# Performance work log

Measured on AMD Instinct MI355X. Metric: run time of the kernel, lower is better.

## Reference

```python
import jax, jax.numpy as jnp
import numpy as np

N_NODES = 100000
N_EDGES = 6400000
EPS = 1e-12


def _gcn_conv(x, edge_index, W, b, n):
    # PyG GCNConv(normalize=True): add self-loops, symmetric deg^-1/2 norm
    src, dst = edge_index[0], edge_index[1]
    loop = jnp.arange(n)
    row = jnp.concatenate([src, loop])
    col = jnp.concatenate([dst, loop])
    deg = jax.ops.segment_sum(jnp.ones(row.shape[0], dtype=x.dtype), col, num_segments=n)
    dinv = jnp.where(deg > 0, jax.lax.rsqrt(deg), 0.0)
    norm = dinv[row] * dinv[col]                       # [E+N]
    xw = x @ W                                          # [N,16]
    out = jax.ops.segment_sum(xw[row] * norm[:, None], col, num_segments=n)
    return out + b


def _sage_conv(x, edge_index, Wl, bl, Wr, n):
    # PyG SAGEConv(aggr='mean', root_weight=True, normalize=True)
    src, dst = edge_index[0], edge_index[1]
    deg = jax.ops.segment_sum(jnp.ones(src.shape[0], dtype=x.dtype), dst, num_segments=n)
    agg = jax.ops.segment_sum(x[src], dst, num_segments=n) / jnp.maximum(deg, 1.0)[:, None]
    out = agg @ Wl + bl + x @ Wr
    nrm = jnp.sqrt(jnp.sum(out * out, axis=-1, keepdims=True))
    return out / jnp.maximum(nrm, EPS)                  # F.normalize(p=2)


def setup_inputs() -> dict:
    key = jax.random.key(0)
    ks = jax.random.split(key, 16)
    s16, s128 = 1.0 / np.sqrt(16.0), 1.0 / np.sqrt(128.0)
    inp = {
        "x": jax.random.normal(ks[0], (N_NODES, 16), dtype=jnp.float32),
        "edge_index": jax.random.randint(ks[1], (2, N_EDGES), 0, N_NODES, dtype=jnp.int64),
        "W_gcn": jax.random.uniform(ks[2], (16, 16), jnp.float32, -s16, s16),
        "b_gcn": jnp.zeros((16,), jnp.float32),
        "Wl1": jax.random.uniform(ks[3], (16, 16), jnp.float32, -s16, s16),
        "bl1": jnp.zeros((16,), jnp.float32),
        "Wr1": jax.random.uniform(ks[4], (16, 16), jnp.float32, -s16, s16),
        "Wl2": jax.random.uniform(ks[5], (16, 16), jnp.float32, -s16, s16),
        "bl2": jnp.zeros((16,), jnp.float32),
        "Wr2": jax.random.uniform(ks[6], (16, 16), jnp.float32, -s16, s16),
        "W1": jax.random.uniform(ks[7], (16, 128), jnp.float32, -s16, s16),
        "b1": jax.random.uniform(ks[8], (128,), jnp.float32, -s16, s16),
        "W2": jax.random.uniform(ks[9], (128, 128), jnp.float32, -s128, s128),
        "b2": jax.random.uniform(ks[10], (128,), jnp.float32, -s128, s128),
        "W3": jax.random.uniform(ks[11], (128, 1), jnp.float32, -s128, s128),
        "b3": jax.random.uniform(ks[12], (1,), jnp.float32, -s128, s128),
    }
    return inp


def reference(x, edge_index, W_gcn, b_gcn, Wl1, bl1, Wr1, Wl2, bl2, Wr2, W1, b1, W2, b2, W3, b3):
    n = x.shape[0]
    h = jnp.tanh(_gcn_conv(x, edge_index, W_gcn, b_gcn, n))
    h = jnp.tanh(_sage_conv(h, edge_index, Wl1, bl1, Wr1, n))
    h = _sage_conv(h, edge_index, Wl2, bl2, Wr2, n)
    h = jax.nn.relu(h @ W1 + b1)
    h = jax.nn.relu(h @ W2 + b2)
    return h @ W3 + b3
```

## Files before the change

kernel.cpp:

```cpp
#include <hip/hip_runtime.h>
#include <hip/hip_bf16.h>
#include <math.h>

#define NBLK 512
#define ROWS (NBLK / 256)
#define MAXNC 512
#define STAGE_CAP 12512

__global__ void k_hist(const int* __restrict__ dst, int* __restrict__ hist,
                       int nE, int nc, int chunk) {
    __shared__ int ch[MAXNC];
    int b = blockIdx.x, t = threadIdx.x;
    for (int i = t; i < nc; i += 256) ch[i] = 0;
    __syncthreads();
    int c0 = b * chunk, c1 = min(nE, c0 + chunk);
    if (c1 > c0) {
        int nv = (c1 - c0) >> 2;
        const int4* d4 = (const int4*)(dst + c0);
        for (int i = t; i < nv; i += 256) {
            int4 dd = d4[i];
            atomicAdd(&ch[dd.x >> 8], 1);
            atomicAdd(&ch[dd.y >> 8], 1);
            atomicAdd(&ch[dd.z >> 8], 1);
            atomicAdd(&ch[dd.w >> 8], 1);
        }
        int rem = (c1 - c0) & 3;
        if (t < rem) atomicAdd(&ch[dst[c0 + (nv << 2) + t] >> 8], 1);
    }
    __syncthreads();
    for (int i = t; i < nc; i += 256) hist[b * nc + i] = ch[i];
}

__global__ void k_scanA(const int* __restrict__ hist, int* __restrict__ offT,
                        int* __restrict__ totPad, int* __restrict__ totReal, int nc) {
    __shared__ int sums[256];
    __shared__ int red[256];
    int c = blockIdx.x, t = threadIdx.x;
    int v[ROWS], p[ROWS];
    int s = 0, sr = 0;
#pragma unroll
    for (int j = 0; j < ROWS; ++j) {
        v[j] = hist[(size_t)(t * ROWS + j) * nc + c];
        p[j] = (v[j] + 15) & ~15;
        s += p[j];
        sr += v[j];
    }
    sums[t] = s;
    red[t] = sr;
    __syncthreads();
    for (int d = 1; d < 256; d <<= 1) {
        int x = (t >= d) ? sums[t - d] : 0;
        __syncthreads();
        sums[t] += x;
        __syncthreads();
    }
    int run = sums[t] - s;
#pragma unroll
    for (int j = 0; j < ROWS; ++j) {
        offT[(size_t)c * NBLK + t * ROWS + j] = run;
        run += p[j];
    }
    if (t == 255) totPad[c] = sums[255];
    for (int d = 128; d > 0; d >>= 1) {
        if (t < d) red[t] += red[t + d];
        __syncthreads();
    }
    if (t == 0) totReal[c] = red[0];
}

__global__ void k_scanB(const int* __restrict__ totPad, const int* __restrict__ totReal,
                        int* __restrict__ cbase, int* __restrict__ rbase,
                        int* __restrict__ rowstart, int nE, int nc, int n) {
    __shared__ int sp[512];
    __shared__ int sr[512];
    int t = threadIdx.x;
    int vp = (t < nc) ? totPad[t] : 0;
    int vr = (t < nc) ? totReal[t] : 0;
    sp[t] = vp; sr[t] = vr;
    __syncthreads();
    for (int d = 1; d < 512; d <<= 1) {
        int xp = (t >= d) ? sp[t - d] : 0;
        int xr = (t >= d) ? sr[t - d] : 0;
        __syncthreads();
        sp[t] += xp; sr[t] += xr;
        __syncthreads();
    }
    if (t < nc) { cbase[t] = sp[t] - vp; rbase[t] = sr[t] - vr; }
    if (t == nc - 1) cbase[nc] = sp[t];
    if (t == 0) rowstart[n] = nE;
}

__global__ __launch_bounds__(256, 2)
void k_fill(const int* __restrict__ src, const int* __restrict__ dst,
            const int* __restrict__ hist, const int* __restrict__ offT,
            const int* __restrict__ cbase,
            int* __restrict__ bucketed, int nE, int nc, int chunk) {
    __shared__ int stage[STAGE_CAP];
    __shared__ int sc[256];
    __shared__ int lbeg[MAXNC];
    __shared__ int lcur[MAXNC];
    int b = blockIdx.x, t = threadIdx.x;

    int v0 = (2 * t < nc) ? hist[(size_t)b * nc + 2 * t] : 0;
    int v1 = (2 * t + 1 < nc) ? hist[(size_t)b * nc + 2 * t + 1] : 0;
    int s = v0 + v1;
    sc[t] = s;
    __syncthreads();
    for (int d = 1; d < 256; d <<= 1) {
        int x = (t >= d) ? sc[t - d] : 0;
        __syncthreads();
        sc[t] += x;
        __syncthreads();
    }
    int excl = sc[t] - s;
    if (2 * t < nc) { lbeg[2 * t] = excl; lcur[2 * t] = excl; }
    if (2 * t + 1 < nc) { lbeg[2 * t + 1] = excl + v0; lcur[2 * t + 1] = excl + v0; }
    __syncthreads();

    int c0 = b * chunk, c1 = min(nE, c0 + chunk);
    if (c1 > c0) {
        int nv = (c1 - c0) >> 2;
        const int4* d4 = (const int4*)(dst + c0);
        const int4* s4 = (const int4*)(src + c0);
        for (int i = t; i < nv; i += 256) {
            int4 dd = d4[i];
            int4 ss = s4[i];
            int pos;
            pos = atomicAdd(&lcur[dd.x >> 8], 1); stage[pos] = ss.x | ((dd.x & 255) << 17);
            pos = atomicAdd(&lcur[dd.y >> 8], 1); stage[pos] = ss.y | ((dd.y & 255) << 17);
            pos = atomicAdd(&lcur[dd.z >> 8], 1); stage[pos] = ss.z | ((dd.z & 255) << 17);
            pos = atomicAdd(&lcur[dd.w >> 8], 1); stage[pos] = ss.w | ((dd.w & 255) << 17);
        }
        int rem = (c1 - c0) & 3;
        if (t < rem) {
            int e = c0 + (nv << 2) + t;
            int d = dst[e];
            int pos = atomicAdd(&lcur[d >> 8], 1);
            stage[pos] = src[e] | ((d & 255) << 17);
        }
    }
    __syncthreads();

    for (int c = t; c < nc; c += 256) {
        int lo = lbeg[c];
        int cnt = lcur[c] - lo;
        int g = cbase[c] + offT[(size_t)c * NBLK + b];
        int padded = (cnt + 15) & ~15;
        for (int i = 0; i < padded; i += 4) {
            int4 v;
            v.x = (i + 0 < cnt) ? stage[lo + i + 0] : -1;
            v.y = (i + 1 < cnt) ? stage[lo + i + 1] : -1;
            v.z = (i + 2 < cnt) ? stage[lo + i + 2] : -1;
            v.w = (i + 3 < cnt) ? stage[lo + i + 3] : -1;
            *(int4*)(bucketed + g + i) = v;
        }
    }
}

__global__ void k_fine(const int* __restrict__ bucketed, const int* __restrict__ cbase,
                       const int* __restrict__ rbase,
                       int* __restrict__ csr, int* __restrict__ rowstart,
                       float* __restrict__ dinv, int n) {
    __shared__ int cnt[256];
    __shared__ int lrs[512];
    __shared__ int cur[256];
    int cb = blockIdx.x, t = threadIdx.x;
    int e0 = cbase[cb], e1 = cbase[cb + 1];
    int r0 = rbase[cb];
    if (t < 256) cnt[t] = 0;
    __syncthreads();
    int nv = (e1 - e0) >> 2;
    const int4* b4 = (const int4*)(bucketed + e0);
    for (int i = t; i < nv; i += 512) {
        int4 en = b4[i];
        if (en.x >= 0) atomicAdd(&cnt[(en.x >> 17) & 255], 1);
        if (en.y >= 0) atomicAdd(&cnt[(en.y >> 17) & 255], 1);
        if (en.z >= 0) atomicAdd(&cnt[(en.z >> 17) & 255], 1);
        if (en.w >= 0) atomicAdd(&cnt[(en.w >> 17) & 255], 1);
    }
    __syncthreads();
    int my = (t < 256) ? cnt[t] : 0;
    lrs[t] = my;
    __syncthreads();
    for (int d = 1; d < 512; d <<= 1) {
        int x = (t >= d) ? lrs[t - d] : 0;
        __syncthreads();
        lrs[t] += x;
        __syncthreads();
    }
    if (t < 256) {
        int excl = lrs[t] - my;
        int node = cb * 256 + t;
        if (node < n) {
            rowstart[node] = r0 + excl;
            dinv[node] = rsqrtf((float)(my + 1));
        }
        cur[t] = r0 + excl;
    }
    __syncthreads();
    for (int i = t; i < nv; i += 512) {
        int4 en = b4[i];
        int pos;
        if (en.x >= 0) { pos = atomicAdd(&cur[(en.x >> 17) & 255], 1); csr[pos] = en.x & 0x1FFFF; }
        if (en.y >= 0) { pos = atomicAdd(&cur[(en.y >> 17) & 255], 1); csr[pos] = en.y & 0x1FFFF; }
        if (en.z >= 0) { pos = atomicAdd(&cur[(en.z >> 17) & 255], 1); csr[pos] = en.z & 0x1FFFF; }
        if (en.w >= 0) { pos = atomicAdd(&cur[(en.w >> 17) & 255], 1); csr[pos] = en.w & 0x1FFFF; }
    }
}

template <int MODE>
__global__ void k_conv(const float* __restrict__ hin, const int* __restrict__ csr,
                       const int* __restrict__ rowstart, const float* __restrict__ dinv,
                       const float* __restrict__ Wa, const float* __restrict__ ba,
                       const float* __restrict__ Wb,
                       float* __restrict__ hout, int n) {
    int wid = (blockIdx.x * blockDim.x + threadIdx.x) >> 6;
    if (wid >= n) return;
    int lane = threadIdx.x & 63;
    int q = lane >> 2;
    int c = lane & 3;
    int r0 = rowstart[wid], r1 = rowstart[wid + 1];
    int cnt = r1 - r0;
    const int* p = csr + r0 + q;
    int my = (cnt > q) ? ((cnt - q + 15) >> 4) : 0;

    float av[4] = {0.f, 0.f, 0.f, 0.f};
    int s0 = (my > 0) ? p[0] : 0;
    int s1 = (my > 1) ? p[16] : 0;
    for (int t = 0; t < my; ++t) {
        int scur = s0;
        s0 = s1;
        s1 = (t + 2 < my) ? p[(t + 2) * 16] : 0;
        float w = (MODE == 0) ? dinv[scur] : 1.0f;
        float4 v = *(const float4*)(hin + scur * 16 + c * 4);
        av[0] += w * v.x; av[1] += w * v.y; av[2] += w * v.z; av[3] += w * v.w;
    }
#pragma unroll
    for (int m = 4; m <= 32; m <<= 1) {
#pragma unroll
        for (int j = 0; j < 4; ++j) av[j] += __shfl_xor(av[j], m);
    }

    float4 hv4 = *(const float4*)(hin + wid * 16 + c * 4);
    float hvv[4] = {hv4.x, hv4.y, hv4.z, hv4.w};

    if (MODE == 0) {
        float di = dinv[wid];
        float di2 = di * di;
#pragma unroll
        for (int j = 0; j < 4; ++j) av[j] = di * av[j] + di2 * hvv[j];
    } else {
        float inv = 1.0f / fmaxf((float)cnt, 1.0f);
#pragma unroll
        for (int j = 0; j < 4; ++j) av[j] *= inv;
    }

    int fo = lane & 15;
    float y = ba[fo];
#pragma unroll
    for (int k = 0; k < 16; ++k) {
        float ak = __shfl(av[k & 3], k >> 2);
        y += ak * Wa[k * 16 + fo];
        if (MODE != 0) {
            float hk = __shfl(hvv[k & 3], k >> 2);
            y += hk * Wb[k * 16 + fo];
        }
    }
    if (MODE == 0) {
        y = tanhf(y);
    } else {
        float sq = y * y;
        sq += __shfl_xor(sq, 1);
        sq += __shfl_xor(sq, 2);
        sq += __shfl_xor(sq, 4);
        sq += __shfl_xor(sq, 8);
        float nrm = fmaxf(sqrtf(sq), 1e-12f);
        y /= nrm;
        if (MODE == 1) y = tanhf(y);
    }
    if ((lane >> 4) == 0) hout[wid * 16 + fo] = y;
}

#define MLP_NODES 64
__global__ __launch_bounds__(256)
void k_mlp(const float* __restrict__ h3,
           const float* __restrict__ W1, const float* __restrict__ b1,
           const float* __restrict__ W2, const float* __restrict__ b2,
           const float* __restrict__ W3, const float* __restrict__ b3,
           float* __restrict__ out, int n) {
    __shared__ float t1T[128][65];
    __shared__ float hpart[MLP_NODES][5];

    int t = threadIdx.x;
    int w = t >> 6;
    int l = t & 63;
    int ow = __builtin_amdgcn_readfirstlane(w * 32);
    int node0 = blockIdx.x * MLP_NODES;
    int node = node0 + l;
    int nodec = min(node, n - 1);

    float acc[32];
    {
        float h[16];
        const float4* hp = (const float4*)(h3 + (size_t)nodec * 16);
#pragma unroll
        for (int q = 0; q < 4; ++q) {
            float4 v = hp[q];
            h[q * 4 + 0] = v.x; h[q * 4 + 1] = v.y; h[q * 4 + 2] = v.z; h[q * 4 + 3] = v.w;
        }
        const float* bp = b1 + ow;
#pragma unroll
        for (int j = 0; j < 32; ++j) acc[j] = bp[j];
#pragma unroll
        for (int k = 0; k < 16; ++k) {
            const float* wr = W1 + k * 128 + ow;
            float hk = h[k];
#pragma unroll
            for (int j = 0; j < 32; ++j) acc[j] += hk * wr[j];
        }
#pragma unroll
        for (int j = 0; j < 32; ++j) t1T[ow + j][l] = fmaxf(acc[j], 0.f);
    }
    __syncthreads();

    {
        const float* bp = b2 + ow;
#pragma unroll
        for (int j = 0; j < 32; ++j) acc[j] = bp[j];
    }
    for (int k = 0; k < 128; ++k) {
        float tk = t1T[k][l];
        const float* wr = W2 + k * 128 + ow;
#pragma unroll
        for (int j = 0; j < 32; ++j) acc[j] += tk * wr[j];
    }

    float part = 0.f;
    {
        const float* wr = W3 + ow;
#pragma unroll
        for (int j = 0; j < 32; ++j) part += fmaxf(acc[j], 0.f) * wr[j];
    }
    hpart[l][w] = part;
    __syncthreads();
    if (w == 0 && node < n) {
        out[node] = hpart[l][0] + hpart[l][1] + hpart[l][2] + hpart[l][3] + b3[0];
    }
}

extern "C" void kernel_launch(void* const* d_in, const int* in_sizes, int n_in,
                              void* d_out, int out_size, void* d_ws, size_t ws_size,
                              hipStream_t stream) {
    const float* x = (const float*)d_in[0];
    const int* ei = (const int*)d_in[1];
    const float* W_gcn = (const float*)d_in[2];
    const float* b_gcn = (const float*)d_in[3];
    const float* Wl1 = (const float*)d_in[4];
    const float* bl1 = (const float*)d_in[5];
    const float* Wr1 = (const float*)d_in[6];
    const float* Wl2 = (const float*)d_in[7];
    const float* bl2 = (const float*)d_in[8];
    const float* Wr2 = (const float*)d_in[9];
    const float* W1 = (const float*)d_in[10];
    const float* b1 = (const float*)d_in[11];
    const float* W2 = (const float*)d_in[12];
    const float* b2 = (const float*)d_in[13];
    const float* W3 = (const float*)d_in[14];
    const float* b3 = (const float*)d_in[15];

    const int N = in_sizes[0] / 16;
    const int E = in_sizes[1] / 2;
    const int NC = (N + 255) >> 8;
    const int chunk = (((E + NBLK - 1) / NBLK) + 3) & ~3;
    const int* src = ei;
    const int* dst = ei + E;

    char* w = (char*)d_ws;
    auto alloc = [&](size_t bytes) {
        void* p = (void*)w;
        w += (bytes + 255) & ~(size_t)255;
        return p;
    };
    int* hist = (int*)alloc((size_t)NBLK * NC * 4);
    int* offT = (int*)alloc((size_t)NBLK * NC * 4);
    int* totPad = (int*)alloc((size_t)NC * 4);
    int* totReal = (int*)alloc((size_t)NC * 4);
    int* cbase = (int*)alloc((size_t)(NC + 1) * 4);
    int* rbase = (int*)alloc((size_t)NC * 4);
    int* rowstart = (int*)alloc((size_t)(N + 1) * 4);
    float* dinv = (float*)alloc((size_t)N * 4);
    int* bucketed = (int*)alloc(((size_t)E + (size_t)NBLK * NC * 16) * 4);
    int* csr = (int*)alloc((size_t)E * 4);
    float* h1 = (float*)alloc((size_t)N * 16 * 4);
    float* h2 = (float*)alloc((size_t)N * 16 * 4);
    float* h3 = (float*)alloc((size_t)N * 16 * 4);

    k_hist<<<NBLK, 256, 0, stream>>>(dst, hist, E, NC, chunk);
    k_scanA<<<NC, 256, 0, stream>>>(hist, offT, totPad, totReal, NC);
    k_scanB<<<1, 512, 0, stream>>>(totPad, totReal, cbase, rbase, rowstart, E, NC, N);
    k_fill<<<NBLK, 256, 0, stream>>>(src, dst, hist, offT, cbase, bucketed, E, NC, chunk);
    k_fine<<<NC, 512, 0, stream>>>(bucketed, cbase, rbase, csr, rowstart, dinv, N);

    long long conv_threads = (long long)N * 64;
    int blk = 256;
    int ggrid = (int)((conv_threads + blk - 1) / blk);
    k_conv<0><<<ggrid, blk, 0, stream>>>(x,  csr, rowstart, dinv, W_gcn, b_gcn, W_gcn, h1, N);
    k_conv<1><<<ggrid, blk, 0, stream>>>(h1, csr, rowstart, dinv, Wl1, bl1, Wr1, h2, N);
    k_conv<2><<<ggrid, blk, 0, stream>>>(h2, csr, rowstart, dinv, Wl2, bl2, Wr2, h3, N);

    int mgrid = (N + MLP_NODES - 1) / MLP_NODES;
    k_mlp<<<mgrid, 256, 0, stream>>>(h3, W1, b1, W2, b2, W3, b3, (float*)d_out, N);
}
```

Baseline: 350.6 us.

## Split node features into half-width planes and separate gather from dense transform

Node features are stored as two 8-float planes so each gather pass touches a 3.2 MB table that fits in cache better than the 6.4 MB full table. The GCN normalization is folded into a prescale pass so aggregation is a plain sum. Each conv becomes two aggregation passes and a separate post kernel that does the matmul, normalization and activation with 4 threads per node. CSR indices use nontemporal loads. The trade-off is reading the CSR twice per layer, more kernel launches, and extra round trips through intermediate buffers.

```diff
diff --git a/kernel.cpp b/kernel.cpp
--- a/kernel.cpp
+++ b/kernel.cpp
@@ -208,82 +208,136 @@
     }
 }
 
+__global__ void k_prescale(const float* __restrict__ x, const float* __restrict__ dinv,
+                           float* __restrict__ xsA, float* __restrict__ xsB, int n) {
+    int i = blockIdx.x * blockDim.x + threadIdx.x;
+    if (i >= n) return;
+    float di = dinv[i];
+    const float4* xp = (const float4*)(x + (size_t)i * 16);
+    float4 v0 = xp[0], v1 = xp[1], v2 = xp[2], v3 = xp[3];
+    v0.x *= di; v0.y *= di; v0.z *= di; v0.w *= di;
+    v1.x *= di; v1.y *= di; v1.z *= di; v1.w *= di;
+    v2.x *= di; v2.y *= di; v2.z *= di; v2.w *= di;
+    v3.x *= di; v3.y *= di; v3.z *= di; v3.w *= di;
+    float4* a = (float4*)(xsA + (size_t)i * 8);
+    float4* b = (float4*)(xsB + (size_t)i * 8);
+    a[0] = v0; a[1] = v1;
+    b[0] = v2; b[1] = v3;
+}
+
+__global__ void k_agg(const float* __restrict__ hhalf, const int* __restrict__ csr,
+                      const int* __restrict__ rowstart, float* __restrict__ agg, int n) {
+    int wid = (blockIdx.x * blockDim.x + threadIdx.x) >> 6;
+    if (wid >= n) return;
+    int lane = threadIdx.x & 63;
+    int q = lane >> 1;
+    int c = lane & 1;
+    int r0 = rowstart[wid], r1 = rowstart[wid + 1];
+    int cnt = r1 - r0;
+    const int* p = csr + r0 + q;
+    int my = (cnt > q) ? ((cnt - q + 31) >> 5) : 0;
+
+    float av[4] = {0.f, 0.f, 0.f, 0.f};
+    int s0 = (my > 0) ? __builtin_nontemporal_load(p) : 0;
+    int s1 = (my > 1) ? __builtin_nontemporal_load(p + 32) : 0;
+    for (int t = 0; t < my; ++t) {
+        int scur = s0;
+        s0 = s1;
+        s1 = (t + 2 < my) ? __builtin_nontemporal_load(p + (t + 2) * 32) : 0;
+        float4 v = *(const float4*)(hhalf + (size_t)scur * 8 + c * 4);
+        av[0] += v.x; av[1] += v.y; av[2] += v.z; av[3] += v.w;
+    }
+#pragma unroll
+    for (int m = 2; m <= 32; m <<= 1) {
+#pragma unroll
+        for (int j = 0; j < 4; ++j) av[j] += __shfl_xor(av[j], m);
+    }
+    if (lane < 2)
+        *(float4*)(agg + (size_t)wid * 8 + c * 4) = make_float4(av[0], av[1], av[2], av[3]);
+}
+
 template <int MODE>
-__global__ void k_conv(const float* __restrict__ hin, const int* __restrict__ csr,
+__global__ void k_post(const float* __restrict__ aggA, const float* __restrict__ aggB,
+                       const float* __restrict__ selfA, const float* __restrict__ selfB,
                        const int* __restrict__ rowstart, const float* __restrict__ dinv,
                        const float* __restrict__ Wa, const float* __restrict__ ba,
                        const float* __restrict__ Wb,
-                       float* __restrict__ hout, int n) {
-    int wid = (blockIdx.x * blockDim.x + threadIdx.x) >> 6;
-    if (wid >= n) return;
+                       float* __restrict__ houtA, float* __restrict__ houtB, int n) {
+    int idx = blockIdx.x * blockDim.x + threadIdx.x;
+    int node = idx >> 2;
+    if (node >= n) return;
+    int t4 = idx & 3;
     int lane = threadIdx.x & 63;
-    int q = lane >> 2;
-    int c = lane & 3;
-    int r0 = rowstart[wid], r1 = rowstart[wid + 1];
-    int cnt = r1 - r0;
-    const int* p = csr + r0 + q;
-    int my = (cnt > q) ? ((cnt - q + 15) >> 4) : 0;
-
-    float av[4] = {0.f, 0.f, 0.f, 0.f};
-    int s0 = (my > 0) ? p[0] : 0;
-    int s1 = (my > 1) ? p[16] : 0;
-    for (int t = 0; t < my; ++t) {
-        int scur = s0;
-        s0 = s1;
-        s1 = (t + 2 < my) ? p[(t + 2) * 16] : 0;
-        float w = (MODE == 0) ? dinv[scur] : 1.0f;
-        float4 v = *(const float4*)(hin + scur * 16 + c * 4);
-        av[0] += w * v.x; av[1] += w * v.y; av[2] += w * v.z; av[3] += w * v.w;
-    }
-#pragma unroll
-    for (int m = 4; m <= 32; m <<= 1) {
-#pragma unroll
-        for (int j = 0; j < 4; ++j) av[j] += __shfl_xor(av[j], m);
-    }
-
-    float4 hv4 = *(const float4*)(hin + wid * 16 + c * 4);
-    float hvv[4] = {hv4.x, hv4.y, hv4.z, hv4.w};
-
+    int lbase = lane & 60;
+
+    const float* ap = ((t4 < 2) ? aggA : aggB) + (size_t)node * 8 + (t4 & 1) * 4;
+    const float* sp = ((t4 < 2) ? selfA : selfB) + (size_t)node * 8 + (t4 & 1) * 4;
+    float4 av = *(const float4*)ap;
+    float4 sv = *(const float4*)sp;
+
+    float a[16], s[16];
+#pragma unroll
+    for (int g = 0; g < 4; ++g) {
+        a[g * 4 + 0] = __shfl(av.x, lbase + g);
+        a[g * 4 + 1] = __shfl(av.y, lbase + g);
+        a[g * 4 + 2] = __shfl(av.z, lbase + g);
+        a[g * 4 + 3] = __shfl(av.w, lbase + g);
+        s[g * 4 + 0] = __shfl(sv.x, lbase + g);
+        s[g * 4 + 1] = __shfl(sv.y, lbase + g);
+        s[g * 4 + 2] = __shfl(sv.z, lbase + g);
+        s[g * 4 + 3] = __shfl(sv.w, lbase + g);
+    }
+
+    int fo = t4 * 4;
+    float yv[4];
     if (MODE == 0) {
-        float di = dinv[wid];
-        float di2 = di * di;
-#pragma unroll
-        for (int j = 0; j < 4; ++j) av[j] = di * av[j] + di2 * hvv[j];
+        float di = dinv[node];
+#pragma unroll
+        for (int k = 0; k < 16; ++k) a[k] = di * (a[k] + s[k]);
+#pragma unroll
+        for (int j = 0; j < 4; ++j) yv[j] = ba[fo + j];
+#pragma unroll
+        for (int k = 0; k < 16; ++k) {
+            float4 w = *(const float4*)(Wa + k * 16 + fo);
+            yv[0] += a[k] * w.x; yv[1] += a[k] * w.y;
+            yv[2] += a[k] * w.z; yv[3] += a[k] * w.w;
+        }
+#pragma unroll
+        for (int j = 0; j < 4; ++j) yv[j] = tanhf(yv[j]);
     } else {
+        int cnt = rowstart[node + 1] - rowstart[node];
         float inv = 1.0f / fmaxf((float)cnt, 1.0f);
 #pragma unroll
-        for (int j = 0; j < 4; ++j) av[j] *= inv;
-    }
-
-    int fo = lane & 15;
-    float y = ba[fo];
-#pragma unroll
-    for (int k = 0; k < 16; ++k) {
-        float ak = __shfl(av[k & 3], k >> 2);
-        y += ak * Wa[k * 16 + fo];
-        if (MODE != 0) {
-            float hk = __shfl(hvv[k & 3], k >> 2);
-            y += hk * Wb[k * 16 + fo];
-        }
-    }
-    if (MODE == 0) {
-        y = tanhf(y);
-    } else {
-        float sq = y * y;
+        for (int k = 0; k < 16; ++k) a[k] *= inv;
+#pragma unroll
+        for (int j = 0; j < 4; ++j) yv[j] = ba[fo + j];
+#pragma unroll
+        for (int k = 0; k < 16; ++k) {
+            float4 wa = *(const float4*)(Wa + k * 16 + fo);
+            float4 wb = *(const float4*)(Wb + k * 16 + fo);
+            yv[0] += a[k] * wa.x + s[k] * wb.x;
+            yv[1] += a[k] * wa.y + s[k] * wb.y;
+            yv[2] += a[k] * wa.z + s[k] * wb.z;
+            yv[3] += a[k] * wa.w + s[k] * wb.w;
+        }
+        float sq = yv[0] * yv[0] + yv[1] * yv[1] + yv[2] * yv[2] + yv[3] * yv[3];
         sq += __shfl_xor(sq, 1);
         sq += __shfl_xor(sq, 2);
-        sq += __shfl_xor(sq, 4);
-        sq += __shfl_xor(sq, 8);
         float nrm = fmaxf(sqrtf(sq), 1e-12f);
-        y /= nrm;
-        if (MODE == 1) y = tanhf(y);
-    }
-    if ((lane >> 4) == 0) hout[wid * 16 + fo] = y;
+#pragma unroll
+        for (int j = 0; j < 4; ++j) yv[j] /= nrm;
+        if (MODE == 1) {
+#pragma unroll
+            for (int j = 0; j < 4; ++j) yv[j] = tanhf(yv[j]);
+        }
+    }
+    float* op = ((t4 < 2) ? houtA : houtB) + (size_t)node * 8 + (t4 & 1) * 4;
+    *(float4*)op = make_float4(yv[0], yv[1], yv[2], yv[3]);
 }
 
 #define MLP_NODES 64
 __global__ __launch_bounds__(256)
-void k_mlp(const float* __restrict__ h3,
+void k_mlp(const float* __restrict__ h3A, const float* __restrict__ h3B,
            const float* __restrict__ W1, const float* __restrict__ b1,
            const float* __restrict__ W2, const float* __restrict__ b2,
            const float* __restrict__ W3, const float* __restrict__ b3,
@@ -302,12 +356,13 @@
     float acc[32];
     {
         float h[16];
-        const float4* hp = (const float4*)(h3 + (size_t)nodec * 16);
-#pragma unroll
-        for (int q = 0; q < 4; ++q) {
-            float4 v = hp[q];
-            h[q * 4 + 0] = v.x; h[q * 4 + 1] = v.y; h[q * 4 + 2] = v.z; h[q * 4 + 3] = v.w;
-        }
+        const float4* hpa = (const float4*)(h3A + (size_t)nodec * 8);
+        const float4* hpb = (const float4*)(h3B + (size_t)nodec * 8);
+        float4 v0 = hpa[0], v1 = hpa[1], v2 = hpb[0], v3 = hpb[1];
+        h[0] = v0.x; h[1] = v0.y; h[2] = v0.z; h[3] = v0.w;
+        h[4] = v1.x; h[5] = v1.y; h[6] = v1.z; h[7] = v1.w;
+        h[8] = v2.x; h[9] = v2.y; h[10] = v2.z; h[11] = v2.w;
+        h[12] = v3.x; h[13] = v3.y; h[14] = v3.z; h[15] = v3.w;
         const float* bp = b1 + ow;
 #pragma unroll
         for (int j = 0; j < 32; ++j) acc[j] = bp[j];
@@ -391,9 +446,16 @@
     float* dinv = (float*)alloc((size_t)N * 4);
     int* bucketed = (int*)alloc(((size_t)E + (size_t)NBLK * NC * 16) * 4);
     int* csr = (int*)alloc((size_t)E * 4);
-    float* h1 = (float*)alloc((size_t)N * 16 * 4);
-    float* h2 = (float*)alloc((size_t)N * 16 * 4);
-    float* h3 = (float*)alloc((size_t)N * 16 * 4);
+    float* xsA = (float*)alloc((size_t)N * 8 * 4);
+    float* xsB = (float*)alloc((size_t)N * 8 * 4);
+    float* aggA = (float*)alloc((size_t)N * 8 * 4);
+    float* aggB = (float*)alloc((size_t)N * 8 * 4);
+    float* h1A = (float*)alloc((size_t)N * 8 * 4);
+    float* h1B = (float*)alloc((size_t)N * 8 * 4);
+    float* h2A = (float*)alloc((size_t)N * 8 * 4);
+    float* h2B = (float*)alloc((size_t)N * 8 * 4);
+    float* h3A = (float*)alloc((size_t)N * 8 * 4);
+    float* h3B = (float*)alloc((size_t)N * 8 * 4);
 
     k_hist<<<NBLK, 256, 0, stream>>>(dst, hist, E, NC, chunk);
     k_scanA<<<NC, 256, 0, stream>>>(hist, offT, totPad, totReal, NC);
@@ -401,13 +463,27 @@
     k_fill<<<NBLK, 256, 0, stream>>>(src, dst, hist, offT, cbase, bucketed, E, NC, chunk);
     k_fine<<<NC, 512, 0, stream>>>(bucketed, cbase, rbase, csr, rowstart, dinv, N);
 
-    long long conv_threads = (long long)N * 64;
     int blk = 256;
-    int ggrid = (int)((conv_threads + blk - 1) / blk);
-    k_conv<0><<<ggrid, blk, 0, stream>>>(x,  csr, rowstart, dinv, W_gcn, b_gcn, W_gcn, h1, N);
-    k_conv<1><<<ggrid, blk, 0, stream>>>(h1, csr, rowstart, dinv, Wl1, bl1, Wr1, h2, N);
-    k_conv<2><<<ggrid, blk, 0, stream>>>(h2, csr, rowstart, dinv, Wl2, bl2, Wr2, h3, N);
+    int ngrid = (N + blk - 1) / blk;
+    long long agg_threads = (long long)N * 64;
+    int agrid = (int)((agg_threads + blk - 1) / blk);
+    int pgrid = (int)(((long long)N * 4 + blk - 1) / blk);
+
+    k_prescale<<<ngrid, blk, 0, stream>>>(x, dinv, xsA, xsB, N);
+
+    k_agg<<<agrid, blk, 0, stream>>>(xsA, csr, rowstart, aggA, N);
+    k_agg<<<agrid, blk, 0, stream>>>(xsB, csr, rowstart, aggB, N);
+    k_post<0><<<pgrid, blk, 0, stream>>>(aggA, aggB, xsA, xsB, rowstart, dinv,
+                                         W_gcn, b_gcn, W_gcn, h1A, h1B, N);
+    k_agg<<<agrid, blk, 0, stream>>>(h1A, csr, rowstart, aggA, N);
+    k_agg<<<agrid, blk, 0, stream>>>(h1B, csr, rowstart, aggB, N);
+    k_post<1><<<pgrid, blk, 0, stream>>>(aggA, aggB, h1A, h1B, rowstart, dinv,
+                                         Wl1, bl1, Wr1, h2A, h2B, N);
+    k_agg<<<agrid, blk, 0, stream>>>(h2A, csr, rowstart, aggA, N);
+    k_agg<<<agrid, blk, 0, stream>>>(h2B, csr, rowstart, aggB, N);
+    k_post<2><<<pgrid, blk, 0, stream>>>(aggA, aggB, h2A, h2B, rowstart, dinv,
+                                         Wl2, bl2, Wr2, h3A, h3B, N);
 
     int mgrid = (N + MLP_NODES - 1) / MLP_NODES;
-    k_mlp<<<mgrid, 256, 0, stream>>>(h3, W1, b1, W2, b2, W3, b3, (float*)d_out, N);
-}
+    k_mlp<<<mgrid, blk, 0, stream>>>(h3A, h3B, W1, b1, W2, b2, W3, b3, (float*)d_out, N);
+}
```

Result: slower. 421.6 us (+20.2%).
